# Optimization experiments

Measured on AMD Instinct MI355X. Metric: run time of the kernel, lower is better.

Reference implementation:

```python
import jax, jax.numpy as jnp
import numpy as np

DECAY = 0.6
GAIN = 0.4
LN_EPS = 1e-5


def ema_scan(x, axis):
    # s_t = DECAY*s_{t-1} + GAIN*x_t, s_{-1}=0, along `axis`; vectorized over all other dims
    xm = jnp.moveaxis(x, axis, 0)
    def step(s, xt):
        s = DECAY * s + GAIN * xt
        return s, s
    _, ys = jax.lax.scan(step, jnp.zeros_like(xm[0]), xm)
    return jnp.moveaxis(ys, 0, axis)


def setup_inputs() -> dict:
    key = jax.random.key(0)
    ks = jax.random.split(key, 8)
    B, H, W, D = 8, 96, 96, 192
    C = 2 * D  # inner_dim
    s_in = 1.0 / np.sqrt(D)
    s_out = 1.0 / np.sqrt(C)
    return {
        "x": jax.random.normal(ks[0], (B, H, W, D), dtype=jnp.float32),
        "W_in": jax.random.uniform(ks[1], (D, C), minval=-s_in, maxval=s_in, dtype=jnp.float32),
        "b_in": jax.random.uniform(ks[2], (C,), minval=-s_in, maxval=s_in, dtype=jnp.float32),
        "conv_w": jax.random.uniform(ks[3], (C, 1, 3, 3), minval=-1.0/3.0, maxval=1.0/3.0, dtype=jnp.float32),
        "ln_g": jnp.ones((C,), dtype=jnp.float32),
        "ln_b": jnp.zeros((C,), dtype=jnp.float32),
        "W_out": jax.random.uniform(ks[4], (C, D), minval=-s_out, maxval=s_out, dtype=jnp.float32),
        "b_out": jax.random.uniform(ks[5], (D,), minval=-s_out, maxval=s_out, dtype=jnp.float32),
    }


def reference(x, W_in, b_in, conv_w, ln_g, ln_b, W_out, b_out):
    C = W_in.shape[1]
    # in_proj: [B,H,W,D] -> [B,H,W,C]
    proj = jnp.einsum("bhwd,dc->bhwc", x, W_in) + b_in
    # channels-first for depthwise conv: [B,C,H,W]
    cf = jnp.transpose(proj, (0, 3, 1, 2))
    local = jax.lax.conv_general_dilated(
        cf, conv_w, window_strides=(1, 1), padding="SAME",
        feature_group_count=C,
        dimension_numbers=("NCHW", "OIHW", "NCHW"))
    # four directional EMA scans
    lr = ema_scan(local, 3)
    rl = jnp.flip(ema_scan(jnp.flip(local, 3), 3), 3)
    tb = ema_scan(local, 2)
    bt = jnp.flip(ema_scan(jnp.flip(local, 2), 2), 2)
    mixed = 0.25 * (lr + rl + tb + bt) + local
    # back to channels-last, layernorm over C
    mixed = jnp.transpose(mixed, (0, 2, 3, 1))
    mu = jnp.mean(mixed, axis=-1, keepdims=True)
    var = jnp.mean(jnp.square(mixed - mu), axis=-1, keepdims=True)
    normed = (mixed - mu) * jax.lax.rsqrt(var + LN_EPS) * ln_g + ln_b
    return jnp.einsum("bhwc,cd->bhwd", normed, W_out) + b_out
```

## Files before the change

### kernel.cpp

```cpp
#include <hip/hip_runtime.h>
#include <hip/hip_bf16.h>

#define NB 8
#define NH 96
#define NW 96
#define ND 192
#define NC 384
#define NPOS (NB*NH*NW)

#define DECAY 0.6f
#define GAIN 0.4f
#define D12 2.1767823e-3f
#define D16 2.8211099e-4f
#define D24 4.7383813e-6f

typedef __attribute__((ext_vector_type(8))) short bf16x8;
typedef __attribute__((ext_vector_type(4))) float f32x4;
typedef __attribute__((ext_vector_type(4))) unsigned short us4;

__device__ inline unsigned short f2bf(float f) {
  unsigned u = __float_as_uint(f);
  u += 0x7fff + ((u >> 16) & 1);
  return (unsigned short)(u >> 16);
}
__device__ inline float bf2f(unsigned short u) {
  return __uint_as_float((unsigned)u << 16);
}

__device__ inline void gload16(const void* g, void* l) {
  __builtin_amdgcn_global_load_lds(
      (const __attribute__((address_space(1))) void*)g,
      (__attribute__((address_space(3))) void*)l, 16, 0, 0);
}

__device__ inline f32x4 ldf4(const float* p) {
  return *reinterpret_cast<const f32x4*>(p);
}
__device__ inline f32x4 ldb4(const unsigned short* p) {
  us4 v = *reinterpret_cast<const us4*>(p);
  return (f32x4){bf2f(v.x), bf2f(v.y), bf2f(v.z), bf2f(v.w)};
}
__device__ inline void stb4(unsigned short* p, f32x4 v) {
  us4 o = {f2bf(v[0]), f2bf(v[1]), f2bf(v[2]), f2bf(v[3])};
  *reinterpret_cast<us4*>(p) = o;
}
__device__ inline uint2 pk4(f32x4 v) {
  us4 o = {f2bf(v[0]), f2bf(v[1]), f2bf(v[2]), f2bf(v[3])};
  uint2 r; __builtin_memcpy(&r, &o, 8); return r;
}
__device__ inline f32x4 up4(uint2 p) {
  return (f32x4){__uint_as_float(p.x << 16), __uint_as_float(p.x & 0xffff0000u),
                 __uint_as_float(p.y << 16), __uint_as_float(p.y & 0xffff0000u)};
}
__device__ inline bf16x8 pk8(f32x4 a, f32x4 b) {
  bf16x8 r;
#pragma unroll
  for (int i = 0; i < 4; ++i) {
    r[i]     = (short)f2bf(a[i]);
    r[i + 4] = (short)f2bf(b[i]);
  }
  return r;
}
__device__ inline unsigned mswz(int row, int byteInRow) {
  return (unsigned)(row * 768 + (byteInRow ^ ((row & 7) << 4)));
}

__global__ __launch_bounds__(256) void cvt_w_kernel(
    const float* __restrict__ Wi, const float* __restrict__ Wo,
    unsigned short* __restrict__ WtI, unsigned short* __restrict__ WtO) {
  int idx = blockIdx.x * 256 + threadIdx.x;
  if (idx < ND * NC) {
    int k = idx / NC, c = idx % NC;
    WtI[c * ND + k] = f2bf(Wi[idx]);
  } else {
    int j = idx - ND * NC;
    int k = j / ND, d = j % ND;
    WtO[d * NC + k] = f2bf(Wo[j]);
  }
}

template<int K, int N, int BN>
__global__ __launch_bounds__(256) void gemm_kernel(
    const float* __restrict__ A32,
    const unsigned short* __restrict__ Bt,
    const float* __restrict__ bias,
    unsigned short* __restrict__ C) {
  constexpr int NF = BN / 32;
  __shared__ __align__(16) unsigned short lsA[8192];
  __shared__ __align__(16) unsigned short lsB[4 * BN * 8];

  const int tid = threadIdx.x;
  const int lane = tid & 63;
  const int wid = tid >> 6;
  const int wm = wid >> 1, wn = wid & 1;
  const int kg = lane >> 4, r16 = lane & 15;
  const int m0 = blockIdx.x * 128;
  const int n0 = blockIdx.y * BN;

  const float* srcAf[4]; float* dstAf[4];
  {
    float* lsAf = (float*)lsA;
#pragma unroll
    for (int p = 0; p < 4; ++p) {
      int s = tid + p * 256;
      int row = s >> 3, g = s & 7;
      int gg = g ^ (row & 7);
      srcAf[p] = A32 + (size_t)(m0 + row) * K + gg * 4;
      dstAf[p] = lsAf + s * 4;
    }
  }
  const unsigned short* srcB0 = Bt + (size_t)(n0 + (tid & (BN - 1))) * K + (tid / BN) * 8;
  const int sb1 = tid + 256;
  const unsigned short* srcBh = Bt + (size_t)(n0 + (sb1 & 127)) * K + (sb1 >> 7) * 8;

  int boff[NF];
#pragma unroll
  for (int n = 0; n < NF; ++n)
    boff[n] = (kg * BN + wn * (BN / 2) + n * 16 + r16) * 8;

  f32x4 acc[4][NF];
  float bv[NF];
#pragma unroll
  for (int n = 0; n < NF; ++n) bv[n] = bias[n0 + wn * (BN / 2) + n * 16 + r16];
#pragma unroll
  for (int m = 0; m < 4; ++m)
#pragma unroll
    for (int n = 0; n < NF; ++n)
      acc[m][n] = (f32x4){bv[n], bv[n], bv[n], bv[n]};

  for (int ks = 0; ks < K / 32; ++ks) {
    const int ke = ks * 32;
#pragma unroll
    for (int p = 0; p < 4; ++p) gload16(srcAf[p] + ke, dstAf[p]);
    gload16(srcB0 + ke, &lsB[tid * 8]);
    if constexpr (BN == 128) gload16(srcBh + ke, &lsB[(tid + 256) * 8]);
    __syncthreads();
    bf16x8 af[4], bfr[NF];
    {
      const float* lsAf = (const float*)lsA;
      const int r7 = r16 & 7;
#pragma unroll
      for (int m = 0; m < 4; ++m) {
        const int rowf = wm * 64 + m * 16 + r16;
        const float* rp = lsAf + rowf * 32;
        f32x4 a0 = *reinterpret_cast<const f32x4*>(rp + ((2 * kg) ^ r7) * 4);
        f32x4 a1 = *reinterpret_cast<const f32x4*>(rp + ((2 * kg + 1) ^ r7) * 4);
        af[m] = pk8(a0, a1);
      }
    }
#pragma unroll
    for (int n = 0; n < NF; ++n)
      bfr[n] = *reinterpret_cast<const bf16x8*>(&lsB[boff[n]]);
#pragma unroll
    for (int m = 0; m < 4; ++m)
#pragma unroll
      for (int n = 0; n < NF; ++n)
        acc[m][n] = __builtin_amdgcn_mfma_f32_16x16x32_bf16(af[m], bfr[n], acc[m][n], 0, 0, 0);
    __syncthreads();
  }

#pragma unroll
  for (int m = 0; m < 4; ++m) {
    const int row = m0 + wm * 64 + m * 16 + kg * 4;
#pragma unroll
    for (int n = 0; n < NF; ++n) {
      const int col = n0 + wn * (BN / 2) + n * 16 + r16;
#pragma unroll
      for (int j = 0; j < 4; ++j)
        C[(size_t)(row + j) * N + col] = f2bf(acc[m][n][j]);
    }
  }
}

__global__ __launch_bounds__(576) void dh_kernel(
    const unsigned short* __restrict__ proj, const float* __restrict__ cw,
    unsigned short* __restrict__ loc_t, unsigned short* __restrict__ acc_t) {
  __shared__ f32x4 agf[6][96];
  __shared__ f32x4 agb[6][96];
  const int tid = threadIdx.x;
  const int c4 = tid % 96;
  const int seg = tid / 96;
  const int w0 = seg * 16;
  const int bid = blockIdx.x;
  const int bh = (bid & 7) * NH + (bid >> 3);
  const int h = bh % NH;
  const int b = bh / NH;

  f32x4 raw[9];
  const float* cwp = cw + (size_t)c4 * 36;
#pragma unroll
  for (int i = 0; i < 9; ++i) raw[i] = ldf4(cwp + i * 4);
  f32x4 qq[9];
#pragma unroll
  for (int tap = 0; tap < 9; ++tap)
#pragma unroll
    for (int c = 0; c < 4; ++c)
      qq[tap][c] = raw[(c * 9 + tap) >> 2][(c * 9 + tap) & 3];

  const bool hm = (h > 0), hp = (h < NH - 1);
  const unsigned short* rowm = proj + ((size_t)(bh - 1) * NW) * NC + c4 * 4;
  const unsigned short* rowc = proj + ((size_t)bh * NW) * NC + c4 * 4;
  const unsigned short* rowp = proj + ((size_t)(bh + 1) * NW) * NC + c4 * 4;
  unsigned short* tbase = loc_t + ((size_t)(b * NW + w0) * NH + h) * NC + c4 * 4;
  unsigned short* abase = acc_t + ((size_t)(b * NW + w0) * NH + h) * NC + c4 * 4;
  const size_t wst = (size_t)NH * NC;

  const f32x4 z = {0.f, 0.f, 0.f, 0.f};
  f32x4 colL[3], colC[3], colR[3];
  if (w0 > 0) {
    colL[0] = hm ? ldb4(rowm + (size_t)(w0 - 1) * NC) : z;
    colL[1] = ldb4(rowc + (size_t)(w0 - 1) * NC);
    colL[2] = hp ? ldb4(rowp + (size_t)(w0 - 1) * NC) : z;
  } else { colL[0] = z; colL[1] = z; colL[2] = z; }
  colC[0] = hm ? ldb4(rowm + (size_t)w0 * NC) : z;
  colC[1] = ldb4(rowc + (size_t)w0 * NC);
  colC[2] = hp ? ldb4(rowp + (size_t)w0 * NC) : z;

  uint2 xr[16];
#pragma unroll
  for (int i = 0; i < 16; ++i) {
    const int w = w0 + i;
    if (w + 1 < NW) {
      colR[0] = hm ? ldb4(rowm + (size_t)(w + 1) * NC) : z;
      colR[1] = ldb4(rowc + (size_t)(w + 1) * NC);
      colR[2] = hp ? ldb4(rowp + (size_t)(w + 1) * NC) : z;
    } else { colR[0] = z; colR[1] = z; colR[2] = z; }
    f32x4 a = colL[0] * qq[0] + colC[0] * qq[1] + colR[0] * qq[2]
            + colL[1] * qq[3] + colC[1] * qq[4] + colR[1] * qq[5]
            + colL[2] * qq[6] + colC[2] * qq[7] + colR[2] * qq[8];
    xr[i] = pk4(a);
    *reinterpret_cast<uint2*>(tbase + (size_t)i * wst) = xr[i];
    colL[0] = colC[0]; colL[1] = colC[1]; colL[2] = colC[2];
    colC[0] = colR[0]; colC[1] = colR[1]; colC[2] = colR[2];
  }

  f32x4 Af = z, Ab = z;
#pragma unroll
  for (int i = 0; i < 16; ++i) Af = DECAY * Af + GAIN * up4(xr[i]);
#pragma unroll
  for (int i = 15; i >= 0; --i) Ab = DECAY * Ab + GAIN * up4(xr[i]);
  agf[seg][c4] = Af; agb[seg][c4] = Ab;
  __syncthreads();
  f32x4 Fin = z, Bin = z;
  if (seg >= 1) Fin = agf[seg - 1][c4];
  if (seg >= 2) Fin += D16 * agf[seg - 2][c4];
  if (seg <= 4) Bin = agb[seg + 1][c4];
  if (seg <= 3) Bin += D16 * agb[seg + 2][c4];

  uint2 bwp[16];
  f32x4 Bs = Bin;
#pragma unroll
  for (int i = 15; i >= 0; --i) {
    Bs = DECAY * Bs + GAIN * up4(xr[i]);
    bwp[i] = pk4(Bs);
  }
  f32x4 Fs = Fin;
#pragma unroll
  for (int i = 0; i < 16; ++i) {
    Fs = DECAY * Fs + GAIN * up4(xr[i]);
    stb4(abase + (size_t)i * wst, Fs + up4(bwp[i]));
  }
}

__global__ __launch_bounds__(768) void vgemm_kernel(
    const unsigned short* __restrict__ loc_t, const unsigned short* __restrict__ acc_t,
    const float* __restrict__ g, const float* __restrict__ bb,
    const unsigned short* __restrict__ WtO, const float* __restrict__ bo,
    float* __restrict__ out) {
  __shared__ __align__(16) unsigned short mix[96 * NC];
  __shared__ __align__(16) unsigned short lsB[2][6144];
  f32x4* ag = (f32x4*)mix;
  char* mixc = (char*)mix;
  const int tid = threadIdx.x;
  const int lane = tid & 63;
  const int kg = lane >> 4, r16 = lane & 15;
  const int c4 = tid % 96;
  const int seg = tid / 96;
  const int h0 = seg * 12;
  const int bw = blockIdx.x;

  {
    int d = tid % 192, kgg = tid / 192;
    gload16(WtO + (size_t)d * NC + kgg * 8, &lsB[0][tid * 8]);
  }

  const size_t base = ((size_t)bw * NH + h0) * NC + c4 * 4;
  const unsigned short* lp = loc_t + base;
  const unsigned short* ap = acc_t + base;
  uint2 xr[12], avp[12];
#pragma unroll
  for (int i = 0; i < 12; ++i) xr[i] = *reinterpret_cast<const uint2*>(lp + (size_t)i * NC);
#pragma unroll
  for (int i = 0; i < 12; ++i) avp[i] = *reinterpret_cast<const uint2*>(ap + (size_t)i * NC);

  const f32x4 z = {0.f, 0.f, 0.f, 0.f};
  f32x4 Af = z, Ab = z;
#pragma unroll
  for (int i = 0; i < 12; ++i) Af = DECAY * Af + GAIN * up4(xr[i]);
#pragma unroll
  for (int i = 11; i >= 0; --i) Ab = DECAY * Ab + GAIN * up4(xr[i]);
  ag[seg * 96 + c4] = Af;
  ag[768 + seg * 96 + c4] = Ab;
  __syncthreads();
  f32x4 Fin = z, Bin = z;
  if (seg >= 1) Fin = ag[(seg - 1) * 96 + c4];
  if (seg >= 2) Fin += D12 * ag[(seg - 2) * 96 + c4];
  if (seg >= 3) Fin += D24 * ag[(seg - 3) * 96 + c4];
  if (seg <= 6) Bin = ag[768 + (seg + 1) * 96 + c4];
  if (seg <= 5) Bin += D12 * ag[768 + (seg + 2) * 96 + c4];
  if (seg <= 4) Bin += D24 * ag[768 + (seg + 3) * 96 + c4];
  __syncthreads();

  f32x4 Bs = Bin;
#pragma unroll
  for (int i = 11; i >= 0; --i) {
    f32x4 xv = up4(xr[i]);
    Bs = DECAY * Bs + GAIN * xv;
    f32x4 part = xv + 0.25f * (up4(avp[i]) + Bs);
    stb4((unsigned short*)(mixc + mswz(h0 + i, c4 * 8)), part);
  }
  f32x4 Fs = Fin;
#pragma unroll
  for (int i = 0; i < 12; ++i) {
    Fs = DECAY * Fs + GAIN * up4(xr[i]);
    unsigned short* slot = (unsigned short*)(mixc + mswz(h0 + i, c4 * 8));
    stb4(slot, ldb4(slot) + 0.25f * Fs);
  }
  __syncthreads();

  const int wave = tid >> 6;
  const int cb = lane * 6;
  {
    float gv[6], bv6[6];
#pragma unroll
    for (int i = 0; i < 6; ++i) { gv[i] = g[cb + i]; bv6[i] = bb[cb + i]; }
    for (int h = wave; h < NH; h += 12) {
      ushort2* p0 = (ushort2*)(mixc + mswz(h, lane * 12));
      ushort2* p1 = (ushort2*)(mixc + mswz(h, lane * 12 + 4));
      ushort2* p2 = (ushort2*)(mixc + mswz(h, lane * 12 + 8));
      ushort2 a2 = *p0, b2 = *p1, c2 = *p2;
      float v[6];
      v[0] = bf2f(a2.x); v[1] = bf2f(a2.y);
      v[2] = bf2f(b2.x); v[3] = bf2f(b2.y);
      v[4] = bf2f(c2.x); v[5] = bf2f(c2.y);
      float sm = 0.f, s2 = 0.f;
#pragma unroll
      for (int i = 0; i < 6; ++i) { sm += v[i]; s2 += v[i] * v[i]; }
#pragma unroll
      for (int o = 32; o > 0; o >>= 1) {
        sm += __shfl_xor(sm, o, 64);
        s2 += __shfl_xor(s2, o, 64);
      }
      float mu = sm * (1.f / NC);
      float r = rsqrtf(s2 * (1.f / NC) - mu * mu + 1e-5f);
      unsigned short o6[6];
#pragma unroll
      for (int i = 0; i < 6; ++i)
        o6[i] = f2bf((v[i] - mu) * r * gv[i] + bv6[i]);
      *p0 = (ushort2){o6[0], o6[1]};
      *p1 = (ushort2){o6[2], o6[3]};
      *p2 = (ushort2){o6[4], o6[5]};
    }
  }
  __syncthreads();

  const int wm = wave >> 2, wn = wave & 3;
  f32x4 acc[2][3];
  {
    float bv[3];
#pragma unroll
    for (int n = 0; n < 3; ++n) bv[n] = bo[wn * 48 + n * 16 + r16];
#pragma unroll
    for (int m = 0; m < 2; ++m)
#pragma unroll
      for (int n = 0; n < 3; ++n)
        acc[m][n] = (f32x4){bv[n], bv[n], bv[n], bv[n]};
  }
  for (int ks = 0; ks < 12; ++ks) {
    if (ks < 11) {
      int d = tid % 192, kgg = tid / 192;
      gload16(WtO + (size_t)d * NC + (ks + 1) * 32 + kgg * 8, &lsB[(ks + 1) & 1][tid * 8]);
    }
    const unsigned short* bufp = lsB[ks & 1];
    bf16x8 af[2], bfr[3];
#pragma unroll
    for (int m = 0; m < 2; ++m) {
      const int row = wm * 32 + m * 16 + r16;
      af[m] = *reinterpret_cast<const bf16x8*>(mixc + mswz(row, ks * 64 + kg * 16));
    }
#pragma unroll
    for (int n = 0; n < 3; ++n)
      bfr[n] = *reinterpret_cast<const bf16x8*>(&bufp[(kg * 192 + wn * 48 + n * 16 + r16) * 8]);
#pragma unroll
    for (int m = 0; m < 2; ++m)
#pragma unroll
      for (int n = 0; n < 3; ++n)
        acc[m][n] = __builtin_amdgcn_mfma_f32_16x16x32_bf16(af[m], bfr[n], acc[m][n], 0, 0, 0);
    __syncthreads();
  }

  const int bq = bw / NW, wq = bw % NW;
#pragma unroll
  for (int m = 0; m < 2; ++m) {
    const int hbase = wm * 32 + m * 16 + kg * 4;
#pragma unroll
    for (int n = 0; n < 3; ++n) {
      const int d = wn * 48 + n * 16 + r16;
#pragma unroll
      for (int j = 0; j < 4; ++j)
        out[((size_t)(bq * NH + hbase + j) * NW + wq) * ND + d] = acc[m][n][j];
    }
  }
}

extern "C" void kernel_launch(void* const* d_in, const int* in_sizes, int n_in,
                              void* d_out, int out_size, void* d_ws, size_t ws_size,
                              hipStream_t stream) {
  const float* x    = (const float*)d_in[0];
  const float* W_in = (const float*)d_in[1];
  const float* b_in = (const float*)d_in[2];
  const float* cw   = (const float*)d_in[3];
  const float* ln_g = (const float*)d_in[4];
  const float* ln_b = (const float*)d_in[5];
  const float* W_out= (const float*)d_in[6];
  const float* b_out= (const float*)d_in[7];
  float* out = (float*)d_out;

  unsigned short* wsu   = (unsigned short*)d_ws;
  unsigned short* proj  = wsu;
  unsigned short* loc_t = proj + 28311552;
  unsigned short* acc_t = loc_t + 28311552;
  unsigned short* WtI   = acc_t + 28311552;
  unsigned short* WtO   = WtI + 73728;

  cvt_w_kernel<<<(2 * ND * NC) / 256, 256, 0, stream>>>(W_in, W_out, WtI, WtO);
  {
    dim3 g(NPOS / 128, NC / 128);
    gemm_kernel<ND, NC, 128><<<g, 256, 0, stream>>>(x, WtI, b_in, proj);
  }
  dh_kernel<<<NB * NH, 576, 0, stream>>>(proj, cw, loc_t, acc_t);
  vgemm_kernel<<<NB * NW, 768, 0, stream>>>(loc_t, acc_t, ln_g, ln_b,
                                            WtO, b_out, out);
}
```

Measured before the change: 177.2 us.

## Halve GEMM barrier count with 64-wide K chunks and single-pass scan combine

The output GEMM now stages 64 K-columns of W_out per LDS buffer instead of 32, so the loop has 6 iterations and 6 barriers rather than 12. The vertical scan stores its local forward and backward partial states in registers during the first pass. Once the cross-segment carries are known, it applies them with precomputed decay powers, replacing the second recurrence and the read-modify-write of shared memory. In exchange, LDS use grows by 24 KB, which can lower occupancy, and more values stay live in registers.

```diff
diff --git a/kernel.cpp b/kernel.cpp
--- a/kernel.cpp
+++ b/kernel.cpp
@@ -268,7 +268,7 @@
     const unsigned short* __restrict__ WtO, const float* __restrict__ bo,
     float* __restrict__ out) {
   __shared__ __align__(16) unsigned short mix[96 * NC];
-  __shared__ __align__(16) unsigned short lsB[2][6144];
+  __shared__ __align__(16) unsigned short lsB[2][12288];
   f32x4* ag = (f32x4*)mix;
   char* mixc = (char*)mix;
   const int tid = threadIdx.x;
@@ -282,6 +282,8 @@
   {
     int d = tid % 192, kgg = tid / 192;
     gload16(WtO + (size_t)d * NC + kgg * 8, &lsB[0][tid * 8]);
+    int s2 = tid + 768, d2 = s2 % 192, kg2 = s2 / 192;
+    gload16(WtO + (size_t)d2 * NC + kg2 * 8, &lsB[0][s2 * 8]);
   }
 
   const size_t base = ((size_t)bw * NH + h0) * NC + c4 * 4;
@@ -294,13 +296,20 @@
   for (int i = 0; i < 12; ++i) avp[i] = *reinterpret_cast<const uint2*>(ap + (size_t)i * NC);
 
   const f32x4 z = {0.f, 0.f, 0.f, 0.f};
-  f32x4 Af = z, Ab = z;
-#pragma unroll
-  for (int i = 0; i < 12; ++i) Af = DECAY * Af + GAIN * up4(xr[i]);
-#pragma unroll
-  for (int i = 11; i >= 0; --i) Ab = DECAY * Ab + GAIN * up4(xr[i]);
-  ag[seg * 96 + c4] = Af;
-  ag[768 + seg * 96 + c4] = Ab;
+  uint2 b0[12], s0[12];
+  f32x4 Bs = z, Fs = z;
+#pragma unroll
+  for (int i = 11; i >= 0; --i) {
+    Bs = DECAY * Bs + GAIN * up4(xr[i]);
+    b0[i] = pk4(Bs);
+  }
+#pragma unroll
+  for (int i = 0; i < 12; ++i) {
+    Fs = DECAY * Fs + GAIN * up4(xr[i]);
+    s0[i] = pk4(Fs);
+  }
+  ag[seg * 96 + c4] = Fs;
+  ag[768 + seg * 96 + c4] = Bs;
   __syncthreads();
   f32x4 Fin = z, Bin = z;
   if (seg >= 1) Fin = ag[(seg - 1) * 96 + c4];
@@ -311,20 +320,18 @@
   if (seg <= 4) Bin += D24 * ag[768 + (seg + 3) * 96 + c4];
   __syncthreads();
 
-  f32x4 Bs = Bin;
-#pragma unroll
-  for (int i = 11; i >= 0; --i) {
-    f32x4 xv = up4(xr[i]);
-    Bs = DECAY * Bs + GAIN * xv;
-    f32x4 part = xv + 0.25f * (up4(avp[i]) + Bs);
-    stb4((unsigned short*)(mixc + mswz(h0 + i, c4 * 8)), part);
-  }
-  f32x4 Fs = Fin;
-#pragma unroll
-  for (int i = 0; i < 12; ++i) {
-    Fs = DECAY * Fs + GAIN * up4(xr[i]);
-    unsigned short* slot = (unsigned short*)(mixc + mswz(h0 + i, c4 * 8));
-    stb4(slot, ldb4(slot) + 0.25f * Fs);
+  {
+    const float dpw[12] = {0.6f, 0.36f, 0.216f, 0.1296f, 0.07776f, 0.046656f,
+                           0.0279936f, 0.01679616f, 0.010077696f,
+                           0.0060466176f, 0.0036279706f, 0.0021767823f};
+#pragma unroll
+    for (int i = 0; i < 12; ++i) {
+      f32x4 xv = up4(xr[i]);
+      f32x4 fs = up4(s0[i]) + dpw[i] * Fin;
+      f32x4 bs = up4(b0[i]) + dpw[11 - i] * Bin;
+      f32x4 mx = xv + 0.25f * (up4(avp[i]) + fs + bs);
+      stb4((unsigned short*)(mixc + mswz(h0 + i, c4 * 8)), mx);
+    }
   }
   __syncthreads();
 
@@ -376,26 +383,34 @@
       for (int n = 0; n < 3; ++n)
         acc[m][n] = (f32x4){bv[n], bv[n], bv[n], bv[n]};
   }
-  for (int ks = 0; ks < 12; ++ks) {
-    if (ks < 11) {
+  for (int ck = 0; ck < 6; ++ck) {
+    if (ck < 5) {
+      unsigned short* dst = lsB[(ck + 1) & 1];
       int d = tid % 192, kgg = tid / 192;
-      gload16(WtO + (size_t)d * NC + (ks + 1) * 32 + kgg * 8, &lsB[(ks + 1) & 1][tid * 8]);
-    }
-    const unsigned short* bufp = lsB[ks & 1];
-    bf16x8 af[2], bfr[3];
-#pragma unroll
-    for (int m = 0; m < 2; ++m) {
-      const int row = wm * 32 + m * 16 + r16;
-      af[m] = *reinterpret_cast<const bf16x8*>(mixc + mswz(row, ks * 64 + kg * 16));
-    }
-#pragma unroll
-    for (int n = 0; n < 3; ++n)
-      bfr[n] = *reinterpret_cast<const bf16x8*>(&bufp[(kg * 192 + wn * 48 + n * 16 + r16) * 8]);
-#pragma unroll
-    for (int m = 0; m < 2; ++m)
+      gload16(WtO + (size_t)d * NC + (ck + 1) * 64 + kgg * 8, &dst[tid * 8]);
+      int s2 = tid + 768, d2 = s2 % 192, kg2 = s2 / 192;
+      gload16(WtO + (size_t)d2 * NC + (ck + 1) * 64 + kg2 * 8, &dst[s2 * 8]);
+    }
+    const unsigned short* bufp = lsB[ck & 1];
+#pragma unroll
+    for (int hh = 0; hh < 2; ++hh) {
+      bf16x8 af[2], bfr[3];
+#pragma unroll
+      for (int m = 0; m < 2; ++m) {
+        const int row = wm * 32 + m * 16 + r16;
+        af[m] = *reinterpret_cast<const bf16x8*>(
+            mixc + mswz(row, ck * 128 + hh * 64 + kg * 16));
+      }
 #pragma unroll
       for (int n = 0; n < 3; ++n)
-        acc[m][n] = __builtin_amdgcn_mfma_f32_16x16x32_bf16(af[m], bfr[n], acc[m][n], 0, 0, 0);
+        bfr[n] = *reinterpret_cast<const bf16x8*>(
+            &bufp[((hh * 4 + kg) * 192 + wn * 48 + n * 16 + r16) * 8]);
+#pragma unroll
+      for (int m = 0; m < 2; ++m)
+#pragma unroll
+        for (int n = 0; n < 3; ++n)
+          acc[m][n] = __builtin_amdgcn_mfma_f32_16x16x32_bf16(af[m], bfr[n], acc[m][n], 0, 0, 0);
+    }
     __syncthreads();
   }
 
```

Result: slower. 192.5 us (+8.6%).
